# Kernel tuning notes

Hardware: AMD Instinct MI355X
Metric: run time of the kernel (lower is better)

The kernel has to match this reference:

```python
import jax, jax.numpy as jnp
import numpy as np

B, S, L, H, D, FF, V = 2, 1024, 12, 12, 768, 3072, 50265
DH = D // H
W1 = 256                      # one-sided window (attention_window=512)
MOTIF = (31 + 96 + 80) * 2    # 414
MAXPOS = 4098
EPS = 1e-5
NEG = jnp.float32(-1e9)


def _ln(x, s, b):
    m = jnp.mean(x, -1, keepdims=True)
    v = jnp.mean(jnp.square(x - m), -1, keepdims=True)
    return (x - m) * jax.lax.rsqrt(v + EPS) * s + b


def setup_inputs() -> dict:
    key = jax.random.key(0)
    ks = iter(jax.random.split(key, 48))
    n = lambda *sh: jax.random.normal(next(ks), sh, jnp.float32) * 0.02
    return {
        "input_ids": jax.random.randint(next(ks), (B, S), 0, V),
        "attention_mask": jnp.ones((B, S), jnp.int32),
        "motif_dist": jax.random.uniform(next(ks), (B, MOTIF), dtype=jnp.float32),
        "emb_word": n(V, D), "emb_pos": n(MAXPOS, D), "emb_type": n(1, D),
        "emb_ln_s": jnp.ones((D,)), "emb_ln_b": jnp.zeros((D,)),
        "Wq": n(L, D, D), "bq": jnp.zeros((L, D)),
        "Wk": n(L, D, D), "bk": jnp.zeros((L, D)),
        "Wv": n(L, D, D), "bv": jnp.zeros((L, D)),
        "Wqg": n(L, D, D), "bqg": jnp.zeros((L, D)),
        "Wkg": n(L, D, D), "bkg": jnp.zeros((L, D)),
        "Wvg": n(L, D, D), "bvg": jnp.zeros((L, D)),
        "Wo": n(L, D, D), "bo": jnp.zeros((L, D)),
        "ln1_s": jnp.ones((L, D)), "ln1_b": jnp.zeros((L, D)),
        "Wi": n(L, D, FF), "bi": jnp.zeros((L, FF)),
        "Wo2": n(L, FF, D), "bo2": jnp.zeros((L, D)),
        "ln2_s": jnp.ones((L, D)), "ln2_b": jnp.zeros((L, D)),
        "head_Wd": n(D + MOTIF, D), "head_bd": jnp.zeros((D,)),
        "head_Wp": n(D, 2), "head_bp": jnp.zeros((2,)),
    }


def reference(input_ids, attention_mask, motif_dist, emb_word, emb_pos, emb_type,
              emb_ln_s, emb_ln_b, Wq, bq, Wk, bk, Wv, bv, Wqg, bqg, Wkg, bkg,
              Wvg, bvg, Wo, bo, ln1_s, ln1_b, Wi, bi, Wo2, bo2, ln2_s, ln2_b,
              head_Wd, head_bd, head_Wp, head_bp):
    Bn, Sn = input_ids.shape
    scale = 1.0 / np.sqrt(DH)
    # RoBERTa-style embeddings: positions start at padding_idx+1 = 2
    pos_ids = jnp.arange(Sn) + 2
    x = emb_word[input_ids] + emb_pos[pos_ids][None] + emb_type[0][None, None]
    x = _ln(x, emb_ln_s, emb_ln_b)

    key_valid = attention_mask.astype(bool)[:, None, None, :]      # [B,1,1,S]
    idx = jnp.arange(Sn)
    is_global = idx == 0                                           # default: CLS-only global
    band = jnp.abs(idx[:, None] - idx[None, :]) <= W1
    # local query attends to its sliding window plus all global keys
    local_allowed = (band | is_global[None, :])[None, None] & key_valid

    def heads(t, s):
        return t.reshape(Bn, s, H, DH).transpose(0, 2, 1, 3)       # [B,H,s,DH]

    for l in range(L):
        q = heads(x @ Wq[l] + bq[l], Sn) * scale
        k = heads(x @ Wk[l] + bk[l], Sn)
        v = heads(x @ Wv[l] + bv[l], Sn)
        scores = jnp.einsum('bhid,bhjd->bhij', q, k)
        probs = jax.nn.softmax(jnp.where(local_allowed, scores, NEG), -1)
        out = jnp.einsum('bhij,bhjd->bhid', probs, v)              # [B,H,S,DH]
        # global (CLS) query: full attention using the *_global projections
        qg = heads(x[:, :1] @ Wqg[l] + bqg[l], 1) * scale          # [B,H,1,DH]
        kg = heads(x @ Wkg[l] + bkg[l], Sn)
        vg = heads(x @ Wvg[l] + bvg[l], Sn)
        sg = jnp.einsum('bhid,bhjd->bhij', qg, kg)                 # [B,H,1,S]
        pg = jax.nn.softmax(jnp.where(key_valid, sg, NEG), -1)
        og = jnp.einsum('bhij,bhjd->bhid', pg, vg)                 # [B,H,1,DH]
        out = jnp.concatenate([og, out[:, :, 1:]], axis=2)
        out = out.transpose(0, 2, 1, 3).reshape(Bn, Sn, D)
        x = _ln(x + out @ Wo[l] + bo[l], ln1_s[l], ln1_b[l])
        h = jax.nn.gelu(x @ Wi[l] + bi[l], approximate=False)
        x = _ln(x + h @ Wo2[l] + bo2[l], ln2_s[l], ln2_b[l])

    # classification head: CLS hidden state concat motif distribution
    hcat = jnp.concatenate([x[:, 0, :], motif_dist], axis=-1)
    return jnp.tanh(hcat @ head_Wd + head_bd) @ head_Wp + head_bp
```

## Files before the change

kernel.cpp:

```cpp
#include <hip/hip_runtime.h>
#include <math.h>

typedef unsigned short u16;
typedef __attribute__((ext_vector_type(8))) short short8;
typedef __attribute__((ext_vector_type(4))) float f32x4;

#define BB 2
#define SS 1024
#define LL 12
#define HH 12
#define DD 768
#define FFF 3072
#define MOTIF 414
#define HCAT (DD + MOTIF)
#define W1 256
#define NEGV -1e9f
#define EPS 1e-5f
#define SCALE 0.125f
#define LD5 3840
#define WL_ELE 8257536

__device__ __forceinline__ float bf2f(u16 u) {
    union { unsigned i; float f; } x; x.i = ((unsigned)u) << 16; return x.f;
}
__device__ __forceinline__ u16 f2bf(float f) {
    union { float f; unsigned i; } x; x.f = f;
    unsigned r = x.i + 0x7fffu + ((x.i >> 16) & 1u);
    return (u16)(r >> 16);
}

__device__ __forceinline__ void gld16(const u16* g, u16* l) {
    __builtin_amdgcn_global_load_lds((const __attribute__((address_space(1))) void*)g,
                                     (__attribute__((address_space(3))) void*)l, 16, 0, 0);
}

__device__ __forceinline__ float block_reduce_sum(float v, float* red) {
    int t = threadIdx.x;
    red[t] = v; __syncthreads();
    #pragma unroll
    for (int s = 128; s > 0; s >>= 1) {
        if (t < s) red[t] += red[t + s];
        __syncthreads();
    }
    float r = red[0]; __syncthreads();
    return r;
}

__global__ __launch_bounds__(256) void embed_ln_kernel(
    const int* __restrict__ ids, const float* __restrict__ ew,
    const float* __restrict__ ep, const float* __restrict__ et,
    const float* __restrict__ gs, const float* __restrict__ gb,
    float* __restrict__ X, u16* __restrict__ Xb) {
    __shared__ float red[256];
    int row = blockIdx.x;
    int s = row % SS;
    int id = ids[row];
    int t = threadIdx.x;
    float v[3];
    float sum = 0.f;
    #pragma unroll
    for (int i = 0; i < 3; ++i) {
        int d = t + 256 * i;
        float x = ew[(size_t)id * DD + d] + ep[(size_t)(s + 2) * DD + d] + et[d];
        v[i] = x; sum += x;
    }
    sum = block_reduce_sum(sum, red);
    float m = sum * (1.f / DD);
    float sq = 0.f;
    #pragma unroll
    for (int i = 0; i < 3; ++i) { float c = v[i] - m; sq += c * c; }
    sq = block_reduce_sum(sq, red);
    float inv = rsqrtf(sq * (1.f / DD) + EPS);
    #pragma unroll
    for (int i = 0; i < 3; ++i) {
        int d = t + 256 * i;
        float o = (v[i] - m) * inv * gs[d] + gb[d];
        X[(size_t)row * DD + d] = o;
        Xb[(size_t)row * DD + d] = f2bf(o);
    }
}

__global__ __launch_bounds__(256) void add_ln_kernel(
    float* __restrict__ X, u16* __restrict__ Xb,
    const float* __restrict__ T1, const float* __restrict__ T2, int useT2,
    const float* __restrict__ gs, const float* __restrict__ gb) {
    __shared__ float red[256];
    int row = blockIdx.x;
    int t = threadIdx.x;
    float v[3];
    float sum = 0.f;
    #pragma unroll
    for (int i = 0; i < 3; ++i) {
        int d = t + 256 * i;
        size_t idx = (size_t)row * DD + d;
        float x = X[idx] + T1[idx] + (useT2 ? T2[idx] : 0.f);
        v[i] = x; sum += x;
    }
    sum = block_reduce_sum(sum, red);
    float m = sum * (1.f / DD);
    float sq = 0.f;
    #pragma unroll
    for (int i = 0; i < 3; ++i) { float c = v[i] - m; sq += c * c; }
    sq = block_reduce_sum(sq, red);
    float inv = rsqrtf(sq * (1.f / DD) + EPS);
    #pragma unroll
    for (int i = 0; i < 3; ++i) {
        int d = t + 256 * i;
        float o = (v[i] - m) * inv * gs[d] + gb[d];
        X[(size_t)row * DD + d] = o;
        Xb[(size_t)row * DD + d] = f2bf(o);
    }
}

template <int LAYERED>
__global__ __launch_bounds__(256) void conv_all_kernel(
    const float* __restrict__ Wqp, const float* __restrict__ Wkp,
    const float* __restrict__ Wvp, const float* __restrict__ Wkgp,
    const float* __restrict__ Wvgp, const float* __restrict__ Wop,
    const float* __restrict__ Wip, const float* __restrict__ Wo2p,
    u16* __restrict__ WtBase) {
    __shared__ float Tt[64][33];
    int l = LAYERED ? blockIdx.y : 0;
    size_t oDD = (size_t)l * DD * DD;
    size_t oFF = (size_t)l * DD * FFF;
    u16* Wt6  = WtBase + (size_t)l * WL_ELE;
    u16* Wti  = Wt6 + 6 * DD * DD;
    u16* Wto2 = Wti + FFF * DD;
    int tid = blockIdx.x;
    const float* W; u16* Wt; int Nd, Kd, n0, k0;
    if (tid < 1728) {
        int z = tid / 288, rem = tid % 288;
        const float* w6[6] = {Wqp + oDD, Wkp + oDD, Wvp + oDD, Wkgp + oDD, Wvgp + oDD, Wop + oDD};
        W = w6[z];
        Wt = Wt6 + (size_t)z * DD * DD;
        Nd = DD; Kd = DD; n0 = (rem % 24) * 32; k0 = (rem / 24) * 64;
    } else if (tid < 2880) {
        int i = tid - 1728;
        W = Wip + oFF; Wt = Wti; Nd = FFF; Kd = DD; n0 = (i % 96) * 32; k0 = (i / 96) * 64;
    } else {
        int i = tid - 2880;
        W = Wo2p + oFF; Wt = Wto2; Nd = DD; Kd = FFF; n0 = (i % 24) * 32; k0 = (i / 24) * 64;
    }
    int t = threadIdx.x;
    int r = t >> 3, c = (t & 7) * 4;
    #pragma unroll
    for (int half = 0; half < 2; ++half) {
        float4 v = *(const float4*)(W + (size_t)(k0 + half * 32 + r) * Nd + n0 + c);
        Tt[half * 32 + r][c + 0] = v.x;
        Tt[half * 32 + r][c + 1] = v.y;
        Tt[half * 32 + r][c + 2] = v.z;
        Tt[half * 32 + r][c + 3] = v.w;
    }
    __syncthreads();
    int n = t >> 3, kk = (t & 7) * 8;
    union { uint4 v; u16 e[8]; } wv;
    #pragma unroll
    for (int j = 0; j < 8; ++j) wv.e[j] = f2bf(Tt[kk + j][n]);
    *(uint4*)&Wt[(size_t)(n0 + n) * Kd + k0 + kk] = wv.v;
}

__global__ __launch_bounds__(256) void bcat_kernel(
    const float* __restrict__ bq, const float* __restrict__ bk,
    const float* __restrict__ bv, const float* __restrict__ bkg,
    const float* __restrict__ bvg, float* __restrict__ bcat) {
    int tid = blockIdx.x * 256 + threadIdx.x;
    if (tid >= LL * LD5) return;
    int l = tid / LD5, r = tid % LD5, z = r / DD, j = r % DD;
    const float* src = (z == 0) ? bq : (z == 1) ? bk : (z == 2) ? bv : (z == 3) ? bkg : bvg;
    bcat[tid] = src[l * DD + j];
}

template <int ACT, int OBF>
__global__ __launch_bounds__(256) void gemm_bf16(
    const u16* __restrict__ A, const u16* __restrict__ Bt,
    const float* __restrict__ bias, void* __restrict__ C0, void* __restrict__ C1,
    int M, int N, int K, int Ksplit) {
    __shared__ __align__(16) u16 As[2][128 * 32];
    __shared__ __align__(16) u16 Bs[2][128 * 32];
    int z = blockIdx.z;
    int kbeg = z * Ksplit;
    int kend = kbeg + Ksplit; if (kend > K) kend = K;
    void* Cout = z ? C1 : C0;
    int t = threadIdx.x, lane = t & 63, wv = t >> 6;
    int bm = blockIdx.y * 128, bn = blockIdx.x * 128;
    int wm = wv >> 1, wn = wv & 1;
    int h = lane >> 4, q15 = lane & 15;
    int rA = wv * 32;
    int rr = lane >> 2, s = lane & 3;
    f32x4 acc[4][4];
    #pragma unroll
    for (int i = 0; i < 4; ++i)
        #pragma unroll
        for (int j = 0; j < 4; ++j) { acc[i][j][0] = 0.f; acc[i][j][1] = 0.f; acc[i][j][2] = 0.f; acc[i][j][3] = 0.f; }

    int nk = (kend - kbeg) >> 5;
    #pragma unroll
    for (int op = 0; op < 2; ++op) {
        int rc = rA + op * 16;
        int r = rc + rr;
        gld16(A  + (size_t)(bm + r) * K + kbeg + ((s ^ (r & 3)) * 8), &As[0][rc * 32]);
        gld16(Bt + (size_t)(bn + r) * K + kbeg + ((s ^ (r & 3)) * 8), &Bs[0][rc * 32]);
    }
    __syncthreads();
    int cur = 0;
    for (int i = 0; i < nk; ++i) {
        if (i + 1 < nk) {
            int k0 = kbeg + ((i + 1) << 5);
            #pragma unroll
            for (int op = 0; op < 2; ++op) {
                int rc = rA + op * 16;
                int r = rc + rr;
                gld16(A  + (size_t)(bm + r) * K + k0 + ((s ^ (r & 3)) * 8), &As[cur ^ 1][rc * 32]);
                gld16(Bt + (size_t)(bn + r) * K + k0 + ((s ^ (r & 3)) * 8), &Bs[cur ^ 1][rc * 32]);
            }
        }
        short8 af[4], bfr[4];
        #pragma unroll
        for (int mf = 0; mf < 4; ++mf) {
            int row = wm * 64 + mf * 16 + q15;
            af[mf] = *(const short8*)&As[cur][row * 32 + ((h ^ (row & 3)) * 8)];
        }
        #pragma unroll
        for (int nf = 0; nf < 4; ++nf) {
            int row = wn * 64 + nf * 16 + q15;
            bfr[nf] = *(const short8*)&Bs[cur][row * 32 + ((h ^ (row & 3)) * 8)];
        }
        #pragma unroll
        for (int mf = 0; mf < 4; ++mf)
            #pragma unroll
            for (int nf = 0; nf < 4; ++nf)
                acc[mf][nf] = __builtin_amdgcn_mfma_f32_16x16x32_bf16(af[mf], bfr[nf], acc[mf][nf], 0, 0, 0);
        __syncthreads();
        cur ^= 1;
    }
    float* Cf = (float*)Cout;
    u16*   Cb = (u16*)Cout;
    #pragma unroll
    for (int mf = 0; mf < 4; ++mf) {
        int mbase = bm + wm * 64 + mf * 16 + h * 4;
        #pragma unroll
        for (int nf = 0; nf < 4; ++nf) {
            int n = bn + wn * 64 + nf * 16 + q15;
            float bv = 0.f;
            if (z == 0) bv = bias[n];
            #pragma unroll
            for (int rg = 0; rg < 4; ++rg) {
                float val = acc[mf][nf][rg] + bv;
                if (ACT == 1) val = 0.5f * val * (1.f + erff(val * 0.70710678118654752f));
                if (OBF) Cb[(size_t)(mbase + rg) * N + n] = f2bf(val);
                else     Cf[(size_t)(mbase + rg) * N + n] = val;
            }
        }
    }
}

__global__ __launch_bounds__(256) void attn_local_mfma(
    const u16* __restrict__ QKV, const int* __restrict__ mask,
    u16* __restrict__ AO) {
    __shared__ __align__(16) u16 Qs[64 * 64];
    __shared__ __align__(16) u16 Ks[64 * 64];
    __shared__ __align__(16) u16 Vst[64 * 64];
    __shared__ __align__(16) u16 Pld[4][16 * 64];
    __shared__ float msk[64];
    int bid = blockIdx.x;
    int qt = bid & 15;
    int hh = (bid >> 4) % HH;
    int b  = bid / (16 * HH);
    int t = threadIdx.x, lane = t & 63, wv = t >> 6;
    int h = lane >> 4, q15 = lane & 15;
    int i0 = qt * 64;

    #pragma unroll
    for (int op = 0; op < 2; ++op) {
        int r = wv * 16 + op * 8 + (lane >> 3), s = lane & 7;
        gld16(QKV + (size_t)(b * SS + i0 + r) * LD5 + hh * 64 + ((s ^ (r & 7)) * 8),
              &Qs[(wv * 16 + op * 8) * 64]);
    }
    __syncthreads();
    short8 bq[2];
    {
        int qrow = wv * 16 + q15;
        #pragma unroll
        for (int ks = 0; ks < 2; ++ks)
            bq[ks] = *(const short8*)&Qs[qrow * 64 + (((ks * 4 + h) ^ (qrow & 7)) * 8)];
    }

    float mrun = -3e38f, lrun = 0.f;
    f32x4 o[4];
    #pragma unroll
    for (int nf = 0; nf < 4; ++nf) { o[nf][0] = 0.f; o[nf][1] = 0.f; o[nf][2] = 0.f; o[nf][3] = 0.f; }

    int jlo = i0 - W1; if (jlo < 0) jlo = 0;
    int jend = i0 + 64 + W1; if (jend > SS) jend = SS;
    int hasCLS = (jlo > 0) ? 1 : 0;
    int nt = hasCLS + (jend - jlo) / 64;
    int iq = i0 + wv * 16 + q15;

    for (int tt = 0; tt < nt; ++tt) {
        int base = (hasCLS && tt == 0) ? 0 : jlo + (tt - hasCLS) * 64;
        if (tt > 0) __syncthreads();
        #pragma unroll
        for (int op = 0; op < 2; ++op) {
            int r = wv * 16 + op * 8 + (lane >> 3), s = lane & 7;
            gld16(QKV + (size_t)(b * SS + base + r) * LD5 + 768 + hh * 64 + ((s ^ (r & 7)) * 8),
                  &Ks[(wv * 16 + op * 8) * 64]);
        }
        {
            int k2 = t & 31, dsec = t >> 5;
            const u16* vp = QKV + (size_t)(b * SS + base + 2 * k2) * LD5 + 1536 + hh * 64 + dsec * 8;
            union { uint4 v; u16 e[8]; } r0, r1;
            r0.v = *(const uint4*)vp;
            r1.v = *(const uint4*)(vp + LD5);
            int slot = k2 >> 2;
            #pragma unroll
            for (int j = 0; j < 8; ++j) {
                int d = dsec * 8 + j;
                unsigned val = (unsigned)r0.e[j] | ((unsigned)r1.e[j] << 16);
                *(unsigned*)&Vst[d * 64 + ((slot ^ (d & 7)) * 8) + ((2 * k2) & 7)] = val;
            }
        }
        if (t < 64) msk[t] = (float)mask[b * SS + base + t];
        __syncthreads();

        f32x4 sacc[4];
        #pragma unroll
        for (int kf = 0; kf < 4; ++kf) { sacc[kf][0] = 0.f; sacc[kf][1] = 0.f; sacc[kf][2] = 0.f; sacc[kf][3] = 0.f; }
        #pragma unroll
        for (int ks = 0; ks < 2; ++ks) {
            #pragma unroll
            for (int kf = 0; kf < 4; ++kf) {
                int krow = kf * 16 + q15;
                short8 afr = *(const short8*)&Ks[krow * 64 + (((ks * 4 + h) ^ (krow & 7)) * 8)];
                sacc[kf] = __builtin_amdgcn_mfma_f32_16x16x32_bf16(afr, bq[ks], sacc[kf], 0, 0, 0);
            }
        }
        float pv[4][4];
        float tmax = -3e38f;
        #pragma unroll
        for (int kf = 0; kf < 4; ++kf) {
            #pragma unroll
            for (int rg = 0; rg < 4; ++rg) {
                int kl = kf * 16 + h * 4 + rg;
                int key = base + kl;
                int dj = iq - key; int adj = dj < 0 ? -dj : dj;
                bool valid = ((adj <= W1) || (key == 0)) && (msk[kl] != 0.f);
                float s = valid ? sacc[kf][rg] * SCALE : NEGV;
                pv[kf][rg] = s;
                tmax = fmaxf(tmax, s);
            }
        }
        tmax = fmaxf(tmax, __shfl_xor(tmax, 16));
        tmax = fmaxf(tmax, __shfl_xor(tmax, 32));
        float mnew = fmaxf(mrun, tmax);
        float fac = __expf(mrun - mnew);
        mrun = mnew;
        float psum = 0.f;
        #pragma unroll
        for (int kf = 0; kf < 4; ++kf)
            #pragma unroll
            for (int rg = 0; rg < 4; ++rg) {
                float p = __expf(pv[kf][rg] - mnew);
                pv[kf][rg] = p; psum += p;
            }
        psum += __shfl_xor(psum, 16);
        psum += __shfl_xor(psum, 32);
        lrun = lrun * fac + psum;
        #pragma unroll
        for (int kf = 0; kf < 4; ++kf) {
            unsigned lo = (unsigned)f2bf(pv[kf][0]) | ((unsigned)f2bf(pv[kf][1]) << 16);
            unsigned hi = (unsigned)f2bf(pv[kf][2]) | ((unsigned)f2bf(pv[kf][3]) << 16);
            int slot = 2 * kf + (h >> 1);
            uint2 w; w.x = lo; w.y = hi;
            *(uint2*)&Pld[wv][q15 * 64 + ((slot ^ (q15 & 7)) * 8) + 4 * (h & 1)] = w;
        }
        float fo0 = __shfl(fac, (h * 4 + 0) | (lane & 48));
        float fo1 = __shfl(fac, (h * 4 + 1) | (lane & 48));
        float fo2 = __shfl(fac, (h * 4 + 2) | (lane & 48));
        float fo3 = __shfl(fac, (h * 4 + 3) | (lane & 48));
        #pragma unroll
        for (int nf = 0; nf < 4; ++nf) {
            o[nf][0] *= fo0; o[nf][1] *= fo1; o[nf][2] *= fo2; o[nf][3] *= fo3;
        }
        asm volatile("s_waitcnt lgkmcnt(0)" ::: "memory");
        #pragma unroll
        for (int ks = 0; ks < 2; ++ks) {
            short8 ap = *(const short8*)&Pld[wv][q15 * 64 + (((ks * 4 + h) ^ (q15 & 7)) * 8)];
            #pragma unroll
            for (int nf = 0; nf < 4; ++nf) {
                int d = nf * 16 + q15;
                short8 bvf = *(const short8*)&Vst[d * 64 + (((ks * 4 + h) ^ (d & 7)) * 8)];
                o[nf] = __builtin_amdgcn_mfma_f32_16x16x32_bf16(ap, bvf, o[nf], 0, 0, 0);
            }
        }
    }
    float linv = 1.f / lrun;
    float g0 = __shfl(linv, (h * 4 + 0) | (lane & 48));
    float g1 = __shfl(linv, (h * 4 + 1) | (lane & 48));
    float g2 = __shfl(linv, (h * 4 + 2) | (lane & 48));
    float g3 = __shfl(linv, (h * 4 + 3) | (lane & 48));
    size_t rb = (size_t)(b * SS + i0 + wv * 16 + h * 4);
    #pragma unroll
    for (int nf = 0; nf < 4; ++nf) {
        int d = hh * 64 + nf * 16 + q15;
        AO[(rb + 0) * DD + d] = f2bf(o[nf][0] * g0);
        AO[(rb + 1) * DD + d] = f2bf(o[nf][1] * g1);
        AO[(rb + 2) * DD + d] = f2bf(o[nf][2] * g2);
        AO[(rb + 3) * DD + d] = f2bf(o[nf][3] * g3);
    }
}

__global__ __launch_bounds__(512) void attn_global_kernel(
    const float* __restrict__ Xf, const float* __restrict__ Wqg,
    const float* __restrict__ bqg, const u16* __restrict__ QKV,
    const int* __restrict__ mask, u16* __restrict__ AO) {
    __shared__ float x0[DD];
    __shared__ float qv[64];
    __shared__ float sc[SS];
    __shared__ float red[512];
    __shared__ float part[8][64];
    int b = blockIdx.x / HH, hh = blockIdx.x % HH;
    int t = threadIdx.x;
    for (int i = t; i < DD; i += 512) x0[i] = Xf[(size_t)b * SS * DD + i];
    __syncthreads();
    {
        int d = t & 63, p = t >> 6;
        float acc = 0.f;
        int k0 = p * 96;
        #pragma unroll 8
        for (int k = k0; k < k0 + 96; ++k)
            acc += x0[k] * Wqg[(size_t)k * DD + hh * 64 + d];
        part[p][d] = acc;
    }
    __syncthreads();
    if (t < 64) {
        float s = bqg[hh * 64 + t];
        #pragma unroll
        for (int p = 0; p < 8; ++p) s += part[p][t];
        qv[t] = s * SCALE;
    }
    __syncthreads();
    for (int j = t; j < SS; j += 512) {
        const u16* kp = QKV + (size_t)(b * SS + j) * LD5 + 2304 + hh * 64;
        float acc = 0.f;
        #pragma unroll
        for (int d0 = 0; d0 < 64; d0 += 8) {
            union { uint4 v; u16 e[8]; } u;
            u.v = *(const uint4*)(kp + d0);
            #pragma unroll
            for (int j2 = 0; j2 < 8; ++j2) acc += qv[d0 + j2] * bf2f(u.e[j2]);
        }
        sc[j] = mask[b * SS + j] ? acc : NEGV;
    }
    __syncthreads();
    float mx = fmaxf(sc[t], sc[t + 512]);
    red[t] = mx; __syncthreads();
    #pragma unroll
    for (int s = 256; s > 0; s >>= 1) {
        if (t < s) red[t] = fmaxf(red[t], red[t + s]);
        __syncthreads();
    }
    mx = red[0]; __syncthreads();
    float e0 = __expf(sc[t] - mx), e1 = __expf(sc[t + 512] - mx);
    sc[t] = e0; sc[t + 512] = e1;
    red[t] = e0 + e1; __syncthreads();
    #pragma unroll
    for (int s = 256; s > 0; s >>= 1) {
        if (t < s) red[t] += red[t + s];
        __syncthreads();
    }
    float lsum = red[0]; __syncthreads();
    int g = t >> 6, d = t & 63;
    float acc = 0.f;
    for (int j = g; j < SS; j += 8)
        acc += sc[j] * bf2f(QKV[(size_t)(b * SS + j) * LD5 + 3072 + hh * 64 + d]);
    part[g][d] = acc;
    __syncthreads();
    if (g == 0) {
        float ov = 0.f;
        #pragma unroll
        for (int p = 0; p < 8; ++p) ov += part[p][d];
        AO[(size_t)(b * SS) * DD + hh * 64 + d] = f2bf(ov / lsum);
    }
}

__global__ __launch_bounds__(256) void head1_kernel(
    const float* __restrict__ X, const float* __restrict__ motif,
    const float* __restrict__ Wd, float* __restrict__ hpart) {
    __shared__ float hc[HCAT];
    __shared__ float part[4][64];
    int jb = blockIdx.x, kp = blockIdx.y, b = blockIdx.z;
    int t = threadIdx.x;
    for (int i = t; i < DD; i += 256) hc[i] = X[(size_t)b * SS * DD + i];
    for (int i = t; i < MOTIF; i += 256) hc[DD + i] = motif[(size_t)b * MOTIF + i];
    __syncthreads();
    int j = jb * 64 + (t & 63);
    int sub = t >> 6;
    int k0 = kp * 148 + sub * 37;
    int k1 = k0 + 37; if (k1 > HCAT) k1 = HCAT;
    float acc = 0.f;
    for (int k = k0; k < k1; ++k) acc += hc[k] * Wd[(size_t)k * DD + j];
    part[sub][t & 63] = acc;
    __syncthreads();
    if (sub == 0) {
        int x = t & 63;
        hpart[((size_t)b * 8 + kp) * DD + j] = part[0][x] + part[1][x] + part[2][x] + part[3][x];
    }
}

__global__ __launch_bounds__(256) void head2_kernel(
    const float* __restrict__ hpart, const float* __restrict__ bd,
    const float* __restrict__ Wp, const float* __restrict__ bp,
    float* __restrict__ out) {
    __shared__ float dvs[DD];
    __shared__ float red[256];
    int b = blockIdx.x;
    int t = threadIdx.x;
    for (int j = t; j < DD; j += 256) {
        float s = bd[j];
        #pragma unroll
        for (int kp = 0; kp < 8; ++kp) s += hpart[((size_t)b * 8 + kp) * DD + j];
        dvs[j] = tanhf(s);
    }
    __syncthreads();
    float a0 = 0.f, a1 = 0.f;
    for (int k = t; k < DD; k += 256) {
        a0 += dvs[k] * Wp[k * 2 + 0];
        a1 += dvs[k] * Wp[k * 2 + 1];
    }
    a0 = block_reduce_sum(a0, red);
    a1 = block_reduce_sum(a1, red);
    if (t == 0) {
        out[b * 2 + 0] = a0 + bp[0];
        out[b * 2 + 1] = a1 + bp[1];
    }
}

extern "C" void kernel_launch(void* const* d_in, const int* in_sizes, int n_in,
                              void* d_out, int out_size, void* d_ws, size_t ws_size,
                              hipStream_t stream) {
    const int*   input_ids = (const int*)d_in[0];
    const int*   attn_mask = (const int*)d_in[1];
    const float* motif     = (const float*)d_in[2];
    const float* emb_word  = (const float*)d_in[3];
    const float* emb_pos   = (const float*)d_in[4];
    const float* emb_type  = (const float*)d_in[5];
    const float* emb_ln_s  = (const float*)d_in[6];
    const float* emb_ln_b  = (const float*)d_in[7];
    const float* Wq  = (const float*)d_in[8];
    const float* bq  = (const float*)d_in[9];
    const float* Wk  = (const float*)d_in[10];
    const float* bk  = (const float*)d_in[11];
    const float* Wv  = (const float*)d_in[12];
    const float* bv  = (const float*)d_in[13];
    const float* Wqg = (const float*)d_in[14];
    const float* bqg = (const float*)d_in[15];
    const float* Wkg = (const float*)d_in[16];
    const float* bkg = (const float*)d_in[17];
    const float* Wvg = (const float*)d_in[18];
    const float* bvg = (const float*)d_in[19];
    const float* Wo  = (const float*)d_in[20];
    const float* bo  = (const float*)d_in[21];
    const float* ln1_s = (const float*)d_in[22];
    const float* ln1_b = (const float*)d_in[23];
    const float* Wi  = (const float*)d_in[24];
    const float* bi  = (const float*)d_in[25];
    const float* Wo2 = (const float*)d_in[26];
    const float* bo2 = (const float*)d_in[27];
    const float* ln2_s = (const float*)d_in[28];
    const float* ln2_b = (const float*)d_in[29];
    const float* head_Wd = (const float*)d_in[30];
    const float* head_bd = (const float*)d_in[31];
    const float* head_Wp = (const float*)d_in[32];
    const float* head_bp = (const float*)d_in[33];

    float* out = (float*)d_out;
    char* base = (char*)d_ws;

    float* Xf   = (float*)(base + 0);
    u16*   Xb   = (u16*)  (base + 6291456);
    u16*   QKVb = (u16*)  (base + 9437184);
    u16*   AOb  = (u16*)  (base + 25165824);
    float* T1f  = (float*)(base + 28311552);

    const size_t NEED_BIG  = 57643008;
    const size_t NEED_HUGE = 239308800;
    bool huge = ws_size >= NEED_HUGE;
    bool big  = huge || ws_size >= NEED_BIG;

    float* T2f = big ? (float*)(base + 34603008) : T1f;
    u16* WtAll; float* bcat; float* hpart;
    u16 *Wt6_s = nullptr, *Wti_s = nullptr, *Wto2_s = nullptr;
    if (huge) {
        bcat  = (float*)(base + 40894464);
        hpart = (float*)(base + 41078784);
        WtAll = (u16*)  (base + 41127936);
    } else {
        size_t wbase = big ? 40894464 : 34603008;
        Wt6_s  = (u16*)(base + wbase);
        Wti_s  = (u16*)(base + wbase + 7077888);
        Wto2_s = (u16*)(base + wbase + 11796480);
        bcat   = (float*)(base + wbase + 16515072);
        hpart  = (float*)(base + wbase + 16699392);
        WtAll  = Wt6_s;
    }
    u16* Hb = QKVb;

    const int nrow = BB * SS;
    const int useT2 = big ? 1 : 0;

    embed_ln_kernel<<<nrow, 256, 0, stream>>>(input_ids, emb_word, emb_pos, emb_type,
                                              emb_ln_s, emb_ln_b, Xf, Xb);
    bcat_kernel<<<(LL * LD5 + 255) / 256, 256, 0, stream>>>(bq, bk, bv, bkg, bvg, bcat);
    if (huge)
        conv_all_kernel<1><<<dim3(4032, 12), 256, 0, stream>>>(
            Wq, Wk, Wv, Wkg, Wvg, Wo, Wi, Wo2, WtAll);

    dim3 g5(30, 16, 1);
    dim3 gO(6, 16, big ? 2 : 1);
    dim3 gFF1(24, 16, 1);
    dim3 gFF2(6, 16, big ? 2 : 1);

    for (int l = 0; l < LL; ++l) {
        size_t oDD = (size_t)l * DD * DD;
        u16 *Wt6, *Wti, *Wto2;
        if (huge) {
            Wt6  = WtAll + (size_t)l * WL_ELE;
            Wti  = Wt6 + 6 * DD * DD;
            Wto2 = Wti + FFF * DD;
        } else {
            conv_all_kernel<0><<<dim3(4032, 1), 256, 0, stream>>>(
                Wq + oDD, Wk + oDD, Wv + oDD, Wkg + oDD, Wvg + oDD, Wo + oDD,
                Wi + (size_t)l * DD * FFF, Wo2 + (size_t)l * FFF * DD, Wt6_s);
            Wt6 = Wt6_s; Wti = Wti_s; Wto2 = Wto2_s;
        }

        gemm_bf16<0, 1><<<g5, 256, 0, stream>>>(Xb, Wt6, bcat + l * LD5, QKVb, QKVb,
                                                nrow, LD5, DD, DD);

        attn_local_mfma<<<BB * HH * 16, 256, 0, stream>>>(QKVb, attn_mask, AOb);
        attn_global_kernel<<<BB * HH, 512, 0, stream>>>(Xf, Wqg + oDD, bqg + l * DD,
                                                        QKVb, attn_mask, AOb);

        gemm_bf16<0, 0><<<gO, 256, 0, stream>>>(AOb, Wt6 + 5 * (size_t)DD * DD, bo + l * DD,
                                                T1f, T2f, nrow, DD, DD, big ? 384 : 768);
        add_ln_kernel<<<nrow, 256, 0, stream>>>(Xf, Xb, T1f, T2f, useT2,
                                                ln1_s + l * DD, ln1_b + l * DD);

        gemm_bf16<1, 1><<<gFF1, 256, 0, stream>>>(Xb, Wti, bi + l * FFF, Hb, Hb,
                                                  nrow, FFF, DD, DD);
        gemm_bf16<0, 0><<<gFF2, 256, 0, stream>>>(Hb, Wto2, bo2 + l * DD,
                                                  T1f, T2f, nrow, DD, FFF, big ? 1536 : 3072);
        add_ln_kernel<<<nrow, 256, 0, stream>>>(Xf, Xb, T1f, T2f, useT2,
                                                ln2_s + l * DD, ln2_b + l * DD);
    }

    head1_kernel<<<dim3(12, 8, BB), 256, 0, stream>>>(Xf, motif, head_Wd, hpart);
    head2_kernel<<<BB, 256, 0, stream>>>(hpart, head_bd, head_Wp, head_bp, out);
}
```

Before: 2.675 ms.

## Deepen GEMM prefetch to two stages and use split-K of four

The GEMM main loop now keeps two K-tiles in flight. It waits with an explicit vmcnt and issues the next global-to-LDS load after the fragments are read, so only one barrier pair guards buffer reuse and the last tile is handled in an epilogue. Split-K for the output projection and FFN2 GEMMs rises from 2 to 4 when workspace allows. The partials are stored contiguously and summed in add_ln through a generic loop. This gives the N=768 GEMMs more blocks and hides memory latency better, at the cost of more partial-sum traffic and a larger workspace requirement.

```diff
diff --git a/kernel.cpp b/kernel.cpp
--- a/kernel.cpp
+++ b/kernel.cpp
@@ -82,18 +82,20 @@
 
 __global__ __launch_bounds__(256) void add_ln_kernel(
     float* __restrict__ X, u16* __restrict__ Xb,
-    const float* __restrict__ T1, const float* __restrict__ T2, int useT2,
+    const float* __restrict__ Tbase, int NT,
     const float* __restrict__ gs, const float* __restrict__ gb) {
     __shared__ float red[256];
     int row = blockIdx.x;
     int t = threadIdx.x;
+    const size_t MN = (size_t)BB * SS * DD;
     float v[3];
     float sum = 0.f;
     #pragma unroll
     for (int i = 0; i < 3; ++i) {
         int d = t + 256 * i;
         size_t idx = (size_t)row * DD + d;
-        float x = X[idx] + T1[idx] + (useT2 ? T2[idx] : 0.f);
+        float x = X[idx];
+        for (int p = 0; p < NT; ++p) x += Tbase[p * MN + idx];
         v[i] = x; sum += x;
     }
     sum = block_reduce_sum(sum, red);
@@ -170,23 +172,36 @@
     bcat[tid] = src[l * DD + j];
 }
 
+#define STAGE(j, buf)                                                                   \
+    do {                                                                                \
+        int _k0 = (j) << 5;                                                             \
+        _Pragma("unroll")                                                               \
+        for (int _op = 0; _op < 2; ++_op) {                                             \
+            int _rc = rA + _op * 16;                                                    \
+            int _r = _rc + rr;                                                          \
+            gld16(A  + (size_t)(bm + _r) * K + kbeg + _k0 + ((s4 ^ (_r & 3)) * 8),      \
+                  &As[buf][_rc * 32]);                                                  \
+            gld16(Bt + (size_t)(bn + _r) * K + kbeg + _k0 + ((s4 ^ (_r & 3)) * 8),      \
+                  &Bs[buf][_rc * 32]);                                                  \
+        }                                                                               \
+    } while (0)
+
 template <int ACT, int OBF>
 __global__ __launch_bounds__(256) void gemm_bf16(
     const u16* __restrict__ A, const u16* __restrict__ Bt,
-    const float* __restrict__ bias, void* __restrict__ C0, void* __restrict__ C1,
+    const float* __restrict__ bias, void* __restrict__ Cout,
     int M, int N, int K, int Ksplit) {
     __shared__ __align__(16) u16 As[2][128 * 32];
     __shared__ __align__(16) u16 Bs[2][128 * 32];
     int z = blockIdx.z;
     int kbeg = z * Ksplit;
     int kend = kbeg + Ksplit; if (kend > K) kend = K;
-    void* Cout = z ? C1 : C0;
     int t = threadIdx.x, lane = t & 63, wv = t >> 6;
     int bm = blockIdx.y * 128, bn = blockIdx.x * 128;
     int wm = wv >> 1, wn = wv & 1;
     int h = lane >> 4, q15 = lane & 15;
     int rA = wv * 32;
-    int rr = lane >> 2, s = lane & 3;
+    int rr = lane >> 2, s4 = lane & 3;
     f32x4 acc[4][4];
     #pragma unroll
     for (int i = 0; i < 4; ++i)
@@ -194,26 +209,12 @@
         for (int j = 0; j < 4; ++j) { acc[i][j][0] = 0.f; acc[i][j][1] = 0.f; acc[i][j][2] = 0.f; acc[i][j][3] = 0.f; }
 
     int nk = (kend - kbeg) >> 5;
-    #pragma unroll
-    for (int op = 0; op < 2; ++op) {
-        int rc = rA + op * 16;
-        int r = rc + rr;
-        gld16(A  + (size_t)(bm + r) * K + kbeg + ((s ^ (r & 3)) * 8), &As[0][rc * 32]);
-        gld16(Bt + (size_t)(bn + r) * K + kbeg + ((s ^ (r & 3)) * 8), &Bs[0][rc * 32]);
-    }
-    __syncthreads();
+    STAGE(0, 0);
+    if (nk > 1) STAGE(1, 1);
     int cur = 0;
-    for (int i = 0; i < nk; ++i) {
-        if (i + 1 < nk) {
-            int k0 = kbeg + ((i + 1) << 5);
-            #pragma unroll
-            for (int op = 0; op < 2; ++op) {
-                int rc = rA + op * 16;
-                int r = rc + rr;
-                gld16(A  + (size_t)(bm + r) * K + k0 + ((s ^ (r & 3)) * 8), &As[cur ^ 1][rc * 32]);
-                gld16(Bt + (size_t)(bn + r) * K + k0 + ((s ^ (r & 3)) * 8), &Bs[cur ^ 1][rc * 32]);
-            }
-        }
+    for (int i = 0; i < nk - 1; ++i) {
+        asm volatile("s_waitcnt vmcnt(4)" ::: "memory");
+        __builtin_amdgcn_s_barrier();
         short8 af[4], bfr[4];
         #pragma unroll
         for (int mf = 0; mf < 4; ++mf) {
@@ -225,15 +226,39 @@
             int row = wn * 64 + nf * 16 + q15;
             bfr[nf] = *(const short8*)&Bs[cur][row * 32 + ((h ^ (row & 3)) * 8)];
         }
+        asm volatile("s_waitcnt lgkmcnt(0)" ::: "memory");
+        __builtin_amdgcn_sched_barrier(0);
+        __builtin_amdgcn_s_barrier();
+        __builtin_amdgcn_sched_barrier(0);
+        if (i + 2 < nk) STAGE(i + 2, cur);
         #pragma unroll
         for (int mf = 0; mf < 4; ++mf)
             #pragma unroll
             for (int nf = 0; nf < 4; ++nf)
                 acc[mf][nf] = __builtin_amdgcn_mfma_f32_16x16x32_bf16(af[mf], bfr[nf], acc[mf][nf], 0, 0, 0);
-        __syncthreads();
         cur ^= 1;
     }
-    float* Cf = (float*)Cout;
+    asm volatile("s_waitcnt vmcnt(0)" ::: "memory");
+    __builtin_amdgcn_s_barrier();
+    {
+        short8 af[4], bfr[4];
+        #pragma unroll
+        for (int mf = 0; mf < 4; ++mf) {
+            int row = wm * 64 + mf * 16 + q15;
+            af[mf] = *(const short8*)&As[cur][row * 32 + ((h ^ (row & 3)) * 8)];
+        }
+        #pragma unroll
+        for (int nf = 0; nf < 4; ++nf) {
+            int row = wn * 64 + nf * 16 + q15;
+            bfr[nf] = *(const short8*)&Bs[cur][row * 32 + ((h ^ (row & 3)) * 8)];
+        }
+        #pragma unroll
+        for (int mf = 0; mf < 4; ++mf)
+            #pragma unroll
+            for (int nf = 0; nf < 4; ++nf)
+                acc[mf][nf] = __builtin_amdgcn_mfma_f32_16x16x32_bf16(af[mf], bfr[nf], acc[mf][nf], 0, 0, 0);
+    }
+    float* Cf = (float*)Cout + (size_t)z * M * N;
     u16*   Cb = (u16*)Cout;
     #pragma unroll
     for (int mf = 0; mf < 4; ++mf) {
@@ -582,20 +607,20 @@
     u16*   AOb  = (u16*)  (base + 25165824);
     float* T1f  = (float*)(base + 28311552);
 
-    const size_t NEED_BIG  = 57643008;
-    const size_t NEED_HUGE = 239308800;
+    const size_t NEED_BIG  = 70225920;
+    const size_t NEED_HUGE = 251891712;
     bool huge = ws_size >= NEED_HUGE;
     bool big  = huge || ws_size >= NEED_BIG;
-
-    float* T2f = big ? (float*)(base + 34603008) : T1f;
+    int NT = big ? 4 : 1;
+
     u16* WtAll; float* bcat; float* hpart;
     u16 *Wt6_s = nullptr, *Wti_s = nullptr, *Wto2_s = nullptr;
     if (huge) {
-        bcat  = (float*)(base + 40894464);
-        hpart = (float*)(base + 41078784);
-        WtAll = (u16*)  (base + 41127936);
+        bcat  = (float*)(base + 53477376);
+        hpart = (float*)(base + 53661696);
+        WtAll = (u16*)  (base + 53710848);
     } else {
-        size_t wbase = big ? 40894464 : 34603008;
+        size_t wbase = big ? 53710848 : 34603008;
         Wt6_s  = (u16*)(base + wbase);
         Wti_s  = (u16*)(base + wbase + 7077888);
         Wto2_s = (u16*)(base + wbase + 11796480);
@@ -606,7 +631,6 @@
     u16* Hb = QKVb;
 
     const int nrow = BB * SS;
-    const int useT2 = big ? 1 : 0;
 
     embed_ln_kernel<<<nrow, 256, 0, stream>>>(input_ids, emb_word, emb_pos, emb_type,
                                               emb_ln_s, emb_ln_b, Xf, Xb);
@@ -616,9 +640,9 @@
             Wq, Wk, Wv, Wkg, Wvg, Wo, Wi, Wo2, WtAll);
 
     dim3 g5(30, 16, 1);
-    dim3 gO(6, 16, big ? 2 : 1);
+    dim3 gO(6, 16, NT);
     dim3 gFF1(24, 16, 1);
-    dim3 gFF2(6, 16, big ? 2 : 1);
+    dim3 gFF2(6, 16, NT);
 
     for (int l = 0; l < LL; ++l) {
         size_t oDD = (size_t)l * DD * DD;
@@ -634,7 +658,7 @@
             Wt6 = Wt6_s; Wti = Wti_s; Wto2 = Wto2_s;
         }
 
-        gemm_bf16<0, 1><<<g5, 256, 0, stream>>>(Xb, Wt6, bcat + l * LD5, QKVb, QKVb,
+        gemm_bf16<0, 1><<<g5, 256, 0, stream>>>(Xb, Wt6, bcat + l * LD5, QKVb,
                                                 nrow, LD5, DD, DD);
 
         attn_local_mfma<<<BB * HH * 16, 256, 0, stream>>>(QKVb, attn_mask, AOb);
@@ -642,15 +666,15 @@
                                                         QKVb, attn_mask, AOb);
 
         gemm_bf16<0, 0><<<gO, 256, 0, stream>>>(AOb, Wt6 + 5 * (size_t)DD * DD, bo + l * DD,
-                                                T1f, T2f, nrow, DD, DD, big ? 384 : 768);
-        add_ln_kernel<<<nrow, 256, 0, stream>>>(Xf, Xb, T1f, T2f, useT2,
+                                                T1f, nrow, DD, DD, DD / NT);
+        add_ln_kernel<<<nrow, 256, 0, stream>>>(Xf, Xb, T1f, NT,
                                                 ln1_s + l * DD, ln1_b + l * DD);
 
-        gemm_bf16<1, 1><<<gFF1, 256, 0, stream>>>(Xb, Wti, bi + l * FFF, Hb, Hb,
+        gemm_bf16<1, 1><<<gFF1, 256, 0, stream>>>(Xb, Wti, bi + l * FFF, Hb,
                                                   nrow, FFF, DD, DD);
         gemm_bf16<0, 0><<<gFF2, 256, 0, stream>>>(Hb, Wto2, bo2 + l * DD,
-                                                  T1f, T2f, nrow, DD, FFF, big ? 1536 : 3072);
-        add_ln_kernel<<<nrow, 256, 0, stream>>>(Xf, Xb, T1f, T2f, useT2,
+                                                  T1f, nrow, DD, FFF, FFF / NT);
+        add_ln_kernel<<<nrow, 256, 0, stream>>>(Xf, Xb, T1f, NT,
                                                 ln2_s + l * DD, ln2_b + l * DD);
     }
 
```

Result: faster. 2.409 ms (-10.0%).
